# Performance work log

Measured on AMD Instinct MI355X. Metric: run time of the kernel, lower is better.

The kernel has to match this reference:

```python
import jax, jax.numpy as jnp
import numpy as np


def setup_inputs() -> dict:
    key = jax.random.key(0)
    k1, k2 = jax.random.split(key)
    a_bar = jax.random.normal(k1, (32, 512, 512), dtype=jnp.float32)
    b_bar = jax.random.normal(k2, (32, 512, 512), dtype=jnp.float32)
    return {"a_bar": a_bar, "b_bar": b_bar}


def reference(a_bar, b_bar):
    # e[b,i,j] = <a_bar[b,i,:], b_bar[b,j,:]>
    e = jnp.einsum("bid,bjd->bij", a_bar, b_bar)
    # a_tilde: row softmax (over j) then weighted sum of b rows
    attn_a = jax.nn.softmax(e, axis=2)            # [B, Sa, Sb]
    a_tilde = jnp.einsum("bij,bjd->bid", attn_a, b_bar)
    # b_tilde: column softmax (over i), transposed, times a_bar
    attn_b = jax.nn.softmax(e, axis=1)            # [B, Sa, Sb]
    b_tilde = jnp.einsum("bij,bid->bjd", attn_b, a_bar)
    m_a = jnp.concatenate([a_bar, a_tilde, a_bar - a_tilde, a_bar * a_tilde], axis=-1)
    m_b = jnp.concatenate([b_bar, b_tilde, b_bar - b_tilde, b_bar * b_tilde], axis=-1)
    return (m_a, m_b)
```

## Files before the change

### kernel.cpp

```cpp
#include <hip/hip_runtime.h>
#include <hip/hip_bf16.h>
#include <math.h>

#define B_   32
#define S_   512
#define SxS  (S_ * S_)
#define LOG2E 1.4426950408889634f

using frag_ab = __attribute__((ext_vector_type(8))) short;
using frag_cd = __attribute__((ext_vector_type(4))) float;

__device__ inline short f2bf(float x) {
    __hip_bfloat16 h = __float2bfloat16(x);
    return *reinterpret_cast<short*>(&h);
}
__device__ inline float bf2f(short s) {
    __hip_bfloat16 h = *reinterpret_cast<__hip_bfloat16*>(&s);
    return __bfloat162float(h);
}

__device__ __forceinline__ void async16(const short* g, short* l) {
    __builtin_amdgcn_global_load_lds(
        (const __attribute__((address_space(1))) void*)g,
        (__attribute__((address_space(3))) void*)l,
        16, 0, 0);
}

__global__ __launch_bounds__(256) void k_prep(const float* __restrict__ A,
                                              const float* __restrict__ Bm,
                                              short* __restrict__ PA,
                                              short* __restrict__ PB,
                                              short* __restrict__ Va,
                                              short* __restrict__ Vb)
{
    const int z   = blockIdx.z;
    const int b   = z & 31;
    const int isB = z >> 5;
    const float* X = (isB ? Bm : A) + (size_t)b * SxS;
    short* P  = (isB ? PB : PA) + (size_t)b * (S_ * 1024);
    short* Vp = (isB ? Vb : Va) + (size_t)b * SxS;
    const float scale = isB ? 1.0f : LOG2E;

    const int i0 = blockIdx.y * 64, d0 = blockIdx.x * 64;

    __shared__ short T[64][72];

    const int sl = threadIdx.x & 7;
    const int il = threadIdx.x >> 3;

    #pragma unroll
    for (int p = 0; p < 2; ++p) {
        const int i    = il + 32 * p;
        const int rowg = i0 + i;
        const float* src = X + (size_t)rowg * S_ + d0 + sl * 8;
        const float4 v0 = *(const float4*)(src);
        const float4 v1 = *(const float4*)(src + 4);

        T[sl * 8 + 0][i] = f2bf(v0.x); T[sl * 8 + 1][i] = f2bf(v0.y);
        T[sl * 8 + 2][i] = f2bf(v0.z); T[sl * 8 + 3][i] = f2bf(v0.w);
        T[sl * 8 + 4][i] = f2bf(v1.x); T[sl * 8 + 5][i] = f2bf(v1.y);
        T[sl * 8 + 6][i] = f2bf(v1.z); T[sl * 8 + 7][i] = f2bf(v1.w);

        const float xs[8] = {v0.x, v0.y, v0.z, v0.w, v1.x, v1.y, v1.z, v1.w};
        frag_ab hi, lo;
        #pragma unroll
        for (int j = 0; j < 8; ++j) {
            const float x = xs[j] * scale;
            const short h = f2bf(x);
            hi[j] = h;
            lo[j] = f2bf(x - bf2f(h));
        }
        const int W = (d0 >> 5) + (sl >> 2);
        const int q = sl & 3;
        short* base = P + (size_t)rowg * 1024 + W * 64;
        *(frag_ab*)(base + (((2 * q)     ^ (rowg & 7)) * 8)) = hi;
        *(frag_ab*)(base + (((2 * q + 1) ^ (rowg & 7)) * 8)) = lo;
    }
    __syncthreads();

    const int pc = threadIdx.x & 7, dl = threadIdx.x >> 3;
    #pragma unroll
    for (int p = 0; p < 2; ++p) {
        const int d  = dl + 32 * p;
        const int dg = d0 + d;
        frag_ab t = *(const frag_ab*)&T[d][pc * 8];
        *(frag_ab*)(Vp + (size_t)dg * 512 + i0 + ((pc ^ (dg & 7)) * 8)) = t;
    }
}

__global__ __launch_bounds__(256) void k_gemm_e(const short* __restrict__ PA,
                                                const short* __restrict__ PB,
                                                float* __restrict__ E,
                                                float* __restrict__ Et)
{
    const int lin     = blockIdx.x + (blockIdx.y << 2) + (blockIdx.z << 4);
    const int logical = ((lin & 7) << 6) + (lin >> 3);
    const int b  = logical >> 4;
    const int i0 = ((logical >> 2) & 3) * 128;
    const int j0 = (logical & 3) * 128;

    const short* Ab = PA + (size_t)b * (S_ * 1024);
    const short* Bb = PB + (size_t)b * (S_ * 1024);
    float* Eb  = E  + (size_t)b * SxS;
    float* Etb = Et + (size_t)b * SxS;

    __shared__ __align__(16) short As[128][64];
    __shared__ __align__(16) short Bs[128][64];

    const int tid  = threadIdx.x;
    const int wave = tid >> 6, lane = tid & 63;
    const int wr   = wave >> 1, wc = wave & 1;
    const int q    = lane >> 4, m = lane & 15;
    const int srow = lane >> 3, schunk = lane & 7;

    frag_cd zero = {0.f, 0.f, 0.f, 0.f};
    frag_cd acc[4][4];
    #pragma unroll
    for (int i = 0; i < 4; ++i)
        #pragma unroll
        for (int j = 0; j < 4; ++j) acc[i][j] = zero;

    for (int k0 = 0; k0 < S_; k0 += 32) {
        const int W = k0 >> 5;
        __syncthreads();
        #pragma unroll
        for (int p = 0; p < 4; ++p) {
            const int seg    = wave * 4 + p;
            const int rowg_a = i0 + seg * 8 + srow;
            const int rowg_b = j0 + seg * 8 + srow;
            async16(Ab + (size_t)rowg_a * 1024 + W * 64 + schunk * 8, &As[seg * 8][0]);
            async16(Bb + (size_t)rowg_b * 1024 + W * 64 + schunk * 8, &Bs[seg * 8][0]);
        }
        __syncthreads();

        frag_ab ah[4], al[4], bh[4], bl[4];
        #pragma unroll
        for (int t = 0; t < 4; ++t) {
            const int ra = wr * 64 + t * 16 + m;
            const int rb = wc * 64 + t * 16 + m;
            ah[t] = *(const frag_ab*)&As[ra][((2 * q)     ^ (ra & 7)) * 8];
            al[t] = *(const frag_ab*)&As[ra][((2 * q + 1) ^ (ra & 7)) * 8];
            bh[t] = *(const frag_ab*)&Bs[rb][((2 * q)     ^ (rb & 7)) * 8];
            bl[t] = *(const frag_ab*)&Bs[rb][((2 * q + 1) ^ (rb & 7)) * 8];
        }
        #pragma unroll
        for (int mt = 0; mt < 4; ++mt)
            #pragma unroll
            for (int nt = 0; nt < 4; ++nt) {
                acc[mt][nt] = __builtin_amdgcn_mfma_f32_16x16x32_bf16(ah[mt], bh[nt], acc[mt][nt], 0, 0, 0);
                acc[mt][nt] = __builtin_amdgcn_mfma_f32_16x16x32_bf16(ah[mt], bl[nt], acc[mt][nt], 0, 0, 0);
                acc[mt][nt] = __builtin_amdgcn_mfma_f32_16x16x32_bf16(al[mt], bh[nt], acc[mt][nt], 0, 0, 0);
            }
    }

    #pragma unroll
    for (int mt = 0; mt < 4; ++mt)
        #pragma unroll
        for (int nt = 0; nt < 4; ++nt) {
            const int rb  = i0 + wr * 64 + mt * 16 + q * 4;
            const int col = j0 + wc * 64 + nt * 16 + m;
            float4 v = make_float4(acc[mt][nt][0], acc[mt][nt][1],
                                   acc[mt][nt][2], acc[mt][nt][3]);
            Eb[(size_t)(rb + 0) * S_ + col] = v.x;
            Eb[(size_t)(rb + 1) * S_ + col] = v.y;
            Eb[(size_t)(rb + 2) * S_ + col] = v.z;
            Eb[(size_t)(rb + 3) * S_ + col] = v.w;
            *(float4*)(Etb + (size_t)col * S_ + rb) = v;
        }
}

__global__ __launch_bounds__(256) void k_softp(float* __restrict__ E,
                                               float* __restrict__ Et,
                                               float* __restrict__ rinv,
                                               float* __restrict__ cinv)
{
    float* buf = blockIdx.y ? Et : E;
    float* piv = blockIdx.y ? cinv : rinv;

    const int row  = blockIdx.x * 4 + (threadIdx.x >> 6);
    const int lane = threadIdx.x & 63;
    float* er = buf + (size_t)row * S_;

    const float4 v0 = *(const float4*)(er + lane * 8);
    const float4 v1 = *(const float4*)(er + lane * 8 + 4);
    const float xs[8] = {v0.x, v0.y, v0.z, v0.w, v1.x, v1.y, v1.z, v1.w};

    float m = xs[0];
    #pragma unroll
    for (int j = 1; j < 8; ++j) m = fmaxf(m, xs[j]);
    #pragma unroll
    for (int off = 32; off >= 1; off >>= 1) m = fmaxf(m, __shfl_xor(m, off));

    float p[8], s = 0.f;
    #pragma unroll
    for (int j = 0; j < 8; ++j) { p[j] = exp2f(xs[j] - m); s += p[j]; }
    #pragma unroll
    for (int off = 32; off >= 1; off >>= 1) s += __shfl_xor(s, off);

    frag_ab out;
    #pragma unroll
    for (int j = 0; j < 8; ++j) out[j] = f2bf(p[j]);

    short* pr = (short*)buf + (size_t)row * 1024;
    const int W = lane >> 3, slt = (lane & 7) ^ (row & 7);
    *(frag_ab*)(pr + W * 64 + slt * 8) = out;
    if (lane == 0) piv[row] = 1.0f / s;
}

__global__ __launch_bounds__(256) void k_pv(const float* __restrict__ E,
                                            const float* __restrict__ Et,
                                            const float* __restrict__ rin_,
                                            const float* __restrict__ cin_,
                                            const short* __restrict__ Va,
                                            const short* __restrict__ Vb,
                                            const float* __restrict__ A,
                                            const float* __restrict__ Bm,
                                            float* __restrict__ Ma,
                                            float* __restrict__ Mb)
{
    const int lin     = blockIdx.x + (blockIdx.y << 2) + (blockIdx.z << 4);
    const int logical = ((lin & 7) << 7) + (lin >> 3);
    const int zz   = logical >> 4;
    const int side = zz >> 5, b = zz & 31;
    const int r0 = ((logical >> 2) & 3) * 128, d0 = (logical & 3) * 128;

    const short* Pb  = (const short*)(side ? Et : E) + (size_t)b * (S_ * 1024);
    const float* rib = (side ? cin_ : rin_) + b * S_;
    const short* Vp  = (side ? Va : Vb) + (size_t)b * SxS;
    const float* Xb  = (side ? Bm : A) + (size_t)b * SxS;
    float* Ob = (side ? Mb : Ma) + (size_t)b * S_ * 2048;

    __shared__ __align__(16) short Ps[128][64];
    __shared__ __align__(16) short Vs[128][64];

    const int tid  = threadIdx.x;
    const int wave = tid >> 6, lane = tid & 63;
    const int wr   = wave >> 1, wc = wave & 1;
    const int q    = lane >> 4, m = lane & 15;
    const int srow = lane >> 3, schunk = lane & 7;

    frag_cd zero = {0.f, 0.f, 0.f, 0.f};
    frag_cd acc[4][4];
    #pragma unroll
    for (int i = 0; i < 4; ++i)
        #pragma unroll
        for (int j = 0; j < 4; ++j) acc[i][j] = zero;

    for (int k0 = 0; k0 < S_; k0 += 64) {
        const int W = k0 >> 6;
        __syncthreads();
        #pragma unroll
        for (int p = 0; p < 4; ++p) {
            const int seg = wave * 4 + p;
            async16(Pb + (size_t)(r0 + seg * 8 + srow) * 1024 + W * 64 + schunk * 8,
                    &Ps[seg * 8][0]);
            async16(Vp + (size_t)(d0 + seg * 8 + srow) * 512  + W * 64 + schunk * 8,
                    &Vs[seg * 8][0]);
        }
        __syncthreads();

        #pragma unroll
        for (int kk = 0; kk < 2; ++kk) {
            frag_ab af[4], bfr[4];
            #pragma unroll
            for (int t = 0; t < 4; ++t) {
                const int ra = wr * 64 + t * 16 + m;
                const int rb = wc * 64 + t * 16 + m;
                af[t]  = *(const frag_ab*)&Ps[ra][(((kk * 4 + q) ^ (ra & 7)) * 8)];
                bfr[t] = *(const frag_ab*)&Vs[rb][(((kk * 4 + q) ^ (rb & 7)) * 8)];
            }
            #pragma unroll
            for (int mt = 0; mt < 4; ++mt)
                #pragma unroll
                for (int nt = 0; nt < 4; ++nt)
                    acc[mt][nt] = __builtin_amdgcn_mfma_f32_16x16x32_bf16(af[mt], bfr[nt], acc[mt][nt], 0, 0, 0);
        }
    }

    #pragma unroll
    for (int mt = 0; mt < 4; ++mt)
        #pragma unroll
        for (int nt = 0; nt < 4; ++nt) {
            const int rb  = r0 + wr * 64 + mt * 16 + q * 4;
            const int col = d0 + wc * 64 + nt * 16 + m;
            #pragma unroll
            for (int r = 0; r < 4; ++r) {
                const int row = rb + r;
                const float at = acc[mt][nt][r] * rib[row];
                const float xv = Xb[(size_t)row * S_ + col];
                float* o = Ob + (size_t)row * 2048 + col;
                o[0]    = xv;
                o[512]  = at;
                o[1024] = xv - at;
                o[1536] = xv * at;
            }
        }
}

extern "C" void kernel_launch(void* const* d_in, const int* in_sizes, int n_in,
                              void* d_out, int out_size, void* d_ws, size_t ws_size,
                              hipStream_t stream)
{
    const float* A  = (const float*)d_in[0];
    const float* Bm = (const float*)d_in[1];
    float* Ma = (float*)d_out;
    float* Mb = Ma + (size_t)B_ * S_ * 2048;

    float* E    = (float*)d_ws;
    float* Et   = E + (size_t)B_ * SxS;
    short* Va   = (short*)(Et + (size_t)B_ * SxS);
    short* Vb   = Va + (size_t)B_ * SxS;
    float* rinv = (float*)(Vb + (size_t)B_ * SxS);
    float* cinv = rinv + B_ * S_;

    short* PA = (short*)d_out;
    short* PB = PA + (size_t)B_ * S_ * 1024;

    k_prep  <<<dim3(8, 8, 64), 256, 0, stream>>>(A, Bm, PA, PB, Va, Vb);
    k_gemm_e<<<dim3(4, 4, 32), 256, 0, stream>>>(PA, PB, E, Et);
    k_softp <<<dim3(4096, 2),  256, 0, stream>>>(E, Et, rinv, cinv);
    k_pv    <<<dim3(4, 4, 64), 256, 0, stream>>>(E, Et, rinv, cinv,
                                                 Va, Vb, A, Bm, Ma, Mb);
}
```

Baseline: 469.6 us.

## Fuse row/column softmax into PV kernel and drop transposed score matrix

```diff
diff --git a/kernel.cpp b/kernel.cpp
--- a/kernel.cpp
+++ b/kernel.cpp
@@ -18,6 +18,7 @@
     __hip_bfloat16 h = *reinterpret_cast<__hip_bfloat16*>(&s);
     return __bfloat162float(h);
 }
+__device__ __forceinline__ int swz(int r) { return (r ^ (r >> 3)) & 7; }
 
 __device__ __forceinline__ void async16(const short* g, short* l) {
     __builtin_amdgcn_global_load_lds(
@@ -90,8 +91,7 @@
 
 __global__ __launch_bounds__(256) void k_gemm_e(const short* __restrict__ PA,
                                                 const short* __restrict__ PB,
-                                                float* __restrict__ E,
-                                                float* __restrict__ Et)
+                                                float* __restrict__ E)
 {
     const int lin     = blockIdx.x + (blockIdx.y << 2) + (blockIdx.z << 4);
     const int logical = ((lin & 7) << 6) + (lin >> 3);
@@ -101,8 +101,7 @@
 
     const short* Ab = PA + (size_t)b * (S_ * 1024);
     const short* Bb = PB + (size_t)b * (S_ * 1024);
-    float* Eb  = E  + (size_t)b * SxS;
-    float* Etb = Et + (size_t)b * SxS;
+    float* Eb = E + (size_t)b * SxS;
 
     __shared__ __align__(16) short As[128][64];
     __shared__ __align__(16) short Bs[128][64];
@@ -159,85 +158,159 @@
         for (int nt = 0; nt < 4; ++nt) {
             const int rb  = i0 + wr * 64 + mt * 16 + q * 4;
             const int col = j0 + wc * 64 + nt * 16 + m;
-            float4 v = make_float4(acc[mt][nt][0], acc[mt][nt][1],
-                                   acc[mt][nt][2], acc[mt][nt][3]);
-            Eb[(size_t)(rb + 0) * S_ + col] = v.x;
-            Eb[(size_t)(rb + 1) * S_ + col] = v.y;
-            Eb[(size_t)(rb + 2) * S_ + col] = v.z;
-            Eb[(size_t)(rb + 3) * S_ + col] = v.w;
-            *(float4*)(Etb + (size_t)col * S_ + rb) = v;
-        }
-}
-
-__global__ __launch_bounds__(256) void k_softp(float* __restrict__ E,
-                                               float* __restrict__ Et,
-                                               float* __restrict__ rinv,
-                                               float* __restrict__ cinv)
+            Eb[(size_t)(rb + 0) * S_ + col] = acc[mt][nt][0];
+            Eb[(size_t)(rb + 1) * S_ + col] = acc[mt][nt][1];
+            Eb[(size_t)(rb + 2) * S_ + col] = acc[mt][nt][2];
+            Eb[(size_t)(rb + 3) * S_ + col] = acc[mt][nt][3];
+        }
+}
+
+__global__ __launch_bounds__(512) void k_pv_fused(const float* __restrict__ E,
+                                                  const short* __restrict__ Va,
+                                                  const short* __restrict__ Vb,
+                                                  const float* __restrict__ A,
+                                                  const float* __restrict__ Bm,
+                                                  float* __restrict__ Ma,
+                                                  float* __restrict__ Mb)
 {
-    float* buf = blockIdx.y ? Et : E;
-    float* piv = blockIdx.y ? cinv : rinv;
-
-    const int row  = blockIdx.x * 4 + (threadIdx.x >> 6);
-    const int lane = threadIdx.x & 63;
-    float* er = buf + (size_t)row * S_;
-
-    const float4 v0 = *(const float4*)(er + lane * 8);
-    const float4 v1 = *(const float4*)(er + lane * 8 + 4);
-    const float xs[8] = {v0.x, v0.y, v0.z, v0.w, v1.x, v1.y, v1.z, v1.w};
-
-    float m = xs[0];
-    #pragma unroll
-    for (int j = 1; j < 8; ++j) m = fmaxf(m, xs[j]);
-    #pragma unroll
-    for (int off = 32; off >= 1; off >>= 1) m = fmaxf(m, __shfl_xor(m, off));
-
-    float p[8], s = 0.f;
-    #pragma unroll
-    for (int j = 0; j < 8; ++j) { p[j] = exp2f(xs[j] - m); s += p[j]; }
-    #pragma unroll
-    for (int off = 32; off >= 1; off >>= 1) s += __shfl_xor(s, off);
-
-    frag_ab out;
-    #pragma unroll
-    for (int j = 0; j < 8; ++j) out[j] = f2bf(p[j]);
-
-    short* pr = (short*)buf + (size_t)row * 1024;
-    const int W = lane >> 3, slt = (lane & 7) ^ (row & 7);
-    *(frag_ab*)(pr + W * 64 + slt * 8) = out;
-    if (lane == 0) piv[row] = 1.0f / s;
-}
-
-__global__ __launch_bounds__(256) void k_pv(const float* __restrict__ E,
-                                            const float* __restrict__ Et,
-                                            const float* __restrict__ rin_,
-                                            const float* __restrict__ cin_,
-                                            const short* __restrict__ Va,
-                                            const short* __restrict__ Vb,
-                                            const float* __restrict__ A,
-                                            const float* __restrict__ Bm,
-                                            float* __restrict__ Ma,
-                                            float* __restrict__ Mb)
-{
-    const int lin     = blockIdx.x + (blockIdx.y << 2) + (blockIdx.z << 4);
-    const int logical = ((lin & 7) << 7) + (lin >> 3);
-    const int zz   = logical >> 4;
-    const int side = zz >> 5, b = zz & 31;
-    const int r0 = ((logical >> 2) & 3) * 128, d0 = (logical & 3) * 128;
-
-    const short* Pb  = (const short*)(side ? Et : E) + (size_t)b * (S_ * 1024);
-    const float* rib = (side ? cin_ : rin_) + b * S_;
-    const short* Vp  = (side ? Va : Vb) + (size_t)b * SxS;
+    const int lin     = blockIdx.x;
+    const int logical = ((lin & 7) << 6) + (lin >> 3);
+    const int side = logical >> 8;
+    const int b    = (logical >> 3) & 31;
+    const int s0   = (logical & 7) * 64;
+
+    const float* Eb  = E + (size_t)b * SxS;
+    const short* Vg  = (side ? Va : Vb) + (size_t)b * SxS;
     const float* Xb  = (side ? Bm : A) + (size_t)b * SxS;
     float* Ob = (side ? Mb : Ma) + (size_t)b * S_ * 2048;
 
-    __shared__ __align__(16) short Ps[128][64];
-    __shared__ __align__(16) short Vs[128][64];
-
-    const int tid  = threadIdx.x;
-    const int wave = tid >> 6, lane = tid & 63;
-    const int wr   = wave >> 1, wc = wave & 1;
-    const int q    = lane >> 4, m = lane & 15;
-    const int srow = lane >> 3, schunk = lane & 7;
+    __shared__ __align__(16) short Pl[64][512];
+    __shared__ __align__(16) short Vs[512][64];
+    __shared__ float riS[64];
+    __shared__ float mS[64];
+
+    float* scr  = (float*)&Vs[0][0];
+    float* scr2 = scr + 4096;
+
+    const int tid = threadIdx.x;
+
+    if (side == 0) {
+        const int r = tid >> 3, sub = tid & 7;
+        const float* er = Eb + (size_t)(s0 + r) * S_;
+
+        float mx = -INFINITY;
+        #pragma unroll
+        for (int fi = 0; fi < 8; ++fi) {
+            const float* p = er + sub * 8 + fi * 64;
+            const float4 u  = *(const float4*)p;
+            const float4 u2 = *(const float4*)(p + 4);
+            mx = fmaxf(mx, fmaxf(fmaxf(u.x, u.y), fmaxf(u.z, u.w)));
+            mx = fmaxf(mx, fmaxf(fmaxf(u2.x, u2.y), fmaxf(u2.z, u2.w)));
+        }
+        mx = fmaxf(mx, __shfl_xor(mx, 1));
+        mx = fmaxf(mx, __shfl_xor(mx, 2));
+        mx = fmaxf(mx, __shfl_xor(mx, 4));
+
+        float s = 0.f;
+        const int sl = (sub ^ swz(r)) * 8;
+        #pragma unroll
+        for (int fi = 0; fi < 8; ++fi) {
+            const float* p = er + sub * 8 + fi * 64;
+            const float4 u  = *(const float4*)p;
+            const float4 u2 = *(const float4*)(p + 4);
+            const float xs[8] = {u.x, u.y, u.z, u.w, u2.x, u2.y, u2.z, u2.w};
+            frag_ab pb;
+            #pragma unroll
+            for (int j = 0; j < 8; ++j) {
+                const float pv = exp2f(xs[j] - mx);
+                s += pv;
+                pb[j] = f2bf(pv);
+            }
+            *(frag_ab*)&Pl[r][fi * 64 + sl] = pb;
+        }
+        s += __shfl_xor(s, 1);
+        s += __shfl_xor(s, 2);
+        s += __shfl_xor(s, 4);
+        if (sub == 0) riS[r] = 1.0f / s;
+    } else {
+        const int ib = tid >> 3, sub = tid & 7;
+
+        float pm[8];
+        #pragma unroll
+        for (int c = 0; c < 8; ++c) pm[c] = -INFINITY;
+        #pragma unroll
+        for (int ii = 0; ii < 8; ++ii) {
+            const float* p = Eb + (size_t)(ib * 8 + ii) * S_ + s0 + sub * 8;
+            const float4 u  = *(const float4*)p;
+            const float4 u2 = *(const float4*)(p + 4);
+            pm[0] = fmaxf(pm[0], u.x);  pm[1] = fmaxf(pm[1], u.y);
+            pm[2] = fmaxf(pm[2], u.z);  pm[3] = fmaxf(pm[3], u.w);
+            pm[4] = fmaxf(pm[4], u2.x); pm[5] = fmaxf(pm[5], u2.y);
+            pm[6] = fmaxf(pm[6], u2.z); pm[7] = fmaxf(pm[7], u2.w);
+        }
+        #pragma unroll
+        for (int c = 0; c < 8; ++c) scr[ib * 64 + sub * 8 + c] = pm[c];
+        __syncthreads();
+        {
+            const int col = tid & 63, h = tid >> 6;
+            float v = scr[(h * 8) * 64 + col];
+            #pragma unroll
+            for (int k = 1; k < 8; ++k) v = fmaxf(v, scr[(h * 8 + k) * 64 + col]);
+            scr2[h * 64 + col] = v;
+        }
+        __syncthreads();
+        if (tid < 64) {
+            float v = scr2[tid];
+            #pragma unroll
+            for (int h = 1; h < 8; ++h) v = fmaxf(v, scr2[h * 64 + tid]);
+            mS[tid] = v;
+        }
+        __syncthreads();
+
+        float ps[8];
+        frag_ab pb[8];
+        #pragma unroll
+        for (int c = 0; c < 8; ++c) ps[c] = 0.f;
+        #pragma unroll
+        for (int ii = 0; ii < 8; ++ii) {
+            const float* p = Eb + (size_t)(ib * 8 + ii) * S_ + s0 + sub * 8;
+            const float4 u  = *(const float4*)p;
+            const float4 u2 = *(const float4*)(p + 4);
+            const float xs[8] = {u.x, u.y, u.z, u.w, u2.x, u2.y, u2.z, u2.w};
+            #pragma unroll
+            for (int c = 0; c < 8; ++c) {
+                const float pv = exp2f(xs[c] - mS[sub * 8 + c]);
+                ps[c] += pv;
+                pb[c][ii] = f2bf(pv);
+            }
+        }
+        #pragma unroll
+        for (int c = 0; c < 8; ++c) {
+            const int cl = sub * 8 + c;
+            *(frag_ab*)&Pl[cl][(ib >> 3) * 64 + (((ib & 7) ^ swz(cl)) * 8)] = pb[c];
+        }
+        __syncthreads();
+        #pragma unroll
+        for (int c = 0; c < 8; ++c) scr[ib * 64 + sub * 8 + c] = ps[c];
+        __syncthreads();
+        {
+            const int col = tid & 63, h = tid >> 6;
+            float v = 0.f;
+            #pragma unroll
+            for (int k = 0; k < 8; ++k) v += scr[(h * 8 + k) * 64 + col];
+            scr2[h * 64 + col] = v;
+        }
+        __syncthreads();
+        if (tid < 64) {
+            float v = 0.f;
+            #pragma unroll
+            for (int h = 0; h < 8; ++h) v += scr2[h * 64 + tid];
+            riS[tid] = 1.0f / v;
+        }
+    }
+
+    const int wv = tid >> 6, lane = tid & 63;
+    const int q = lane >> 4, m = lane & 15;
 
     frag_cd zero = {0.f, 0.f, 0.f, 0.f};
     frag_cd acc[4][4];
@@ -247,33 +320,30 @@
         for (int j = 0; j < 4; ++j) acc[i][j] = zero;
 
     for (int k0 = 0; k0 < S_; k0 += 64) {
-        const int W = k0 >> 6;
-        __syncthreads();
-        #pragma unroll
-        for (int p = 0; p < 4; ++p) {
-            const int seg = wave * 4 + p;
-            async16(Pb + (size_t)(r0 + seg * 8 + srow) * 1024 + W * 64 + schunk * 8,
-                    &Ps[seg * 8][0]);
-            async16(Vp + (size_t)(d0 + seg * 8 + srow) * 512  + W * 64 + schunk * 8,
-                    &Vs[seg * 8][0]);
+        __syncthreads();
+        #pragma unroll
+        for (int p = 0; p < 8; ++p) {
+            const int d = p * 64 + wv * 8 + (lane >> 3);
+            async16(Vg + (size_t)d * 512 + k0 + (lane & 7) * 8,
+                    &Vs[p * 64 + wv * 8][0]);
         }
         __syncthreads();
 
         #pragma unroll
         for (int kk = 0; kk < 2; ++kk) {
-            frag_ab af[4], bfr[4];
+            frag_ab af[4], bf[4];
             #pragma unroll
             for (int t = 0; t < 4; ++t) {
-                const int ra = wr * 64 + t * 16 + m;
-                const int rb = wc * 64 + t * 16 + m;
-                af[t]  = *(const frag_ab*)&Ps[ra][(((kk * 4 + q) ^ (ra & 7)) * 8)];
-                bfr[t] = *(const frag_ab*)&Vs[rb][(((kk * 4 + q) ^ (rb & 7)) * 8)];
+                const int row = t * 16 + m;
+                af[t] = *(const frag_ab*)&Pl[row][k0 + (((kk * 4 + q) ^ swz(row)) * 8)];
+                const int dl = wv * 64 + t * 16 + m;
+                bf[t] = *(const frag_ab*)&Vs[dl][(((kk * 4 + q) ^ (dl & 7)) * 8)];
             }
             #pragma unroll
             for (int mt = 0; mt < 4; ++mt)
                 #pragma unroll
                 for (int nt = 0; nt < 4; ++nt)
-                    acc[mt][nt] = __builtin_amdgcn_mfma_f32_16x16x32_bf16(af[mt], bfr[nt], acc[mt][nt], 0, 0, 0);
+                    acc[mt][nt] = __builtin_amdgcn_mfma_f32_16x16x32_bf16(af[mt], bf[nt], acc[mt][nt], 0, 0, 0);
         }
     }
 
@@ -281,14 +351,14 @@
     for (int mt = 0; mt < 4; ++mt)
         #pragma unroll
         for (int nt = 0; nt < 4; ++nt) {
-            const int rb  = r0 + wr * 64 + mt * 16 + q * 4;
-            const int col = d0 + wc * 64 + nt * 16 + m;
-            #pragma unroll
-            for (int r = 0; r < 4; ++r) {
-                const int row = rb + r;
-                const float at = acc[mt][nt][r] * rib[row];
-                const float xv = Xb[(size_t)row * S_ + col];
-                float* o = Ob + (size_t)row * 2048 + col;
+            const int col = wv * 64 + nt * 16 + m;
+            #pragma unroll
+            for (int rr = 0; rr < 4; ++rr) {
+                const int rl   = mt * 16 + q * 4 + rr;
+                const int rowg = s0 + rl;
+                const float at = acc[mt][nt][rr] * riS[rl];
+                const float xv = Xb[(size_t)rowg * S_ + col];
+                float* o = Ob + (size_t)rowg * 2048 + col;
                 o[0]    = xv;
                 o[512]  = at;
                 o[1024] = xv - at;
@@ -306,19 +376,14 @@
     float* Ma = (float*)d_out;
     float* Mb = Ma + (size_t)B_ * S_ * 2048;
 
-    float* E    = (float*)d_ws;
-    float* Et   = E + (size_t)B_ * SxS;
-    short* Va   = (short*)(Et + (size_t)B_ * SxS);
-    short* Vb   = Va + (size_t)B_ * SxS;
-    float* rinv = (float*)(Vb + (size_t)B_ * SxS);
-    float* cinv = rinv + B_ * S_;
+    float* E  = (float*)d_ws;
+    short* Va = (short*)(E + (size_t)B_ * SxS);
+    short* Vb = Va + (size_t)B_ * SxS;
 
     short* PA = (short*)d_out;
     short* PB = PA + (size_t)B_ * S_ * 1024;
 
-    k_prep  <<<dim3(8, 8, 64), 256, 0, stream>>>(A, Bm, PA, PB, Va, Vb);
-    k_gemm_e<<<dim3(4, 4, 32), 256, 0, stream>>>(PA, PB, E, Et);
-    k_softp <<<dim3(4096, 2),  256, 0, stream>>>(E, Et, rinv, cinv);
-    k_pv    <<<dim3(4, 4, 64), 256, 0, stream>>>(E, Et, rinv, cinv,
-                                                 Va, Vb, A, Bm, Ma, Mb);
-}
+    k_prep    <<<dim3(8, 8, 64), 256, 0, stream>>>(A, Bm, PA, PB, Va, Vb);
+    k_gemm_e  <<<dim3(4, 4, 32), 256, 0, stream>>>(PA, PB, E);
+    k_pv_fused<<<dim3(512),      512, 0, stream>>>(E, Va, Vb, A, Bm, Ma, Mb);
+}
```

Result: no change. 468.1 us (-0.3%).
